# Kernel tuning notes

Hardware: AMD Instinct MI355X
Metric: run time of the kernel (lower is better)

Reference implementation:

```python
import jax, jax.numpy as jnp
import numpy as np

B, L, D = 8, 2048, 1024

def setup_inputs() -> dict:
    key = jax.random.key(0)
    ks = jax.random.split(key, 12)
    s = 1.0 / np.sqrt(D)
    return {
        "q": jax.random.normal(ks[0], (B, L, D), jnp.float32),
        "k": jax.random.normal(ks[1], (B, L, D), jnp.float32),
        "v": jax.random.normal(ks[2], (B, L, D), jnp.float32),
        "mask": jnp.ones((B, L), jnp.float32),
        # Linear params stored as [in, out] so y = x @ W + b
        "Wq": jax.random.normal(ks[3], (D, D), jnp.float32) * s,
        "bq": jnp.zeros((D,), jnp.float32),
        "Wk": jax.random.normal(ks[4], (D, D), jnp.float32) * s,
        "bk": jnp.zeros((D,), jnp.float32),
        "Wv": jax.random.normal(ks[5], (D, D), jnp.float32) * s,
        "bv": jnp.zeros((D,), jnp.float32),
        "Wg": jax.random.normal(ks[6], (2 * D, D), jnp.float32) * (1.0 / np.sqrt(2 * D)),
        "bg": jnp.zeros((D,), jnp.float32),
    }

def reference(q, k, v, mask, Wq, bq, Wk, bk, Wv, bv, Wg, bg):
    q0 = q
    qp = q @ Wq + bq          # [B, Lq, D]
    kp = k @ Wk + bk          # [B, Lk, D]
    vp = v @ Wv + bv          # [B, Lk, D]
    scale = 1.0 / jnp.sqrt(jnp.asarray(qp.shape[-1], qp.dtype))
    w = jnp.einsum('bqd,bkd->bqk', qp, kp) * scale
    w = jax.nn.softmax(w, axis=-1)          # dim=2 == last axis for 3-D
    x = jnp.einsum('bqk,bkd->bqd', w, vp)
    gate = jnp.concatenate((qp, x), axis=-1) @ Wg + bg
    x = x * mask[..., None]
    x = x * jax.nn.sigmoid(gate)
    return x + q0  # add=True
```

## Files before the change

kernel.cpp:

```cpp
#include <hip/hip_runtime.h>

typedef unsigned int u32;
typedef unsigned short u16;
using v4f    = __attribute__((ext_vector_type(4))) float;
using short8 = __attribute__((ext_vector_type(8))) short;

#define GAS __attribute__((address_space(1)))
#define LAS __attribute__((address_space(3)))

__device__ __forceinline__ u16 f2bf(float f){
  u32 u = __builtin_bit_cast(u32, f);
  u32 r = (u + 0x7fffu + ((u >> 16) & 1u)) >> 16;
  return (u16)r;
}
__device__ __forceinline__ float bf2f(u16 h){
  u32 u = ((u32)h) << 16;
  return __builtin_bit_cast(float, u);
}

__device__ __forceinline__ void gld_lds16(const void* g, void* l){
  __builtin_amdgcn_global_load_lds((const GAS u32*)g, (LAS u32*)l, 16, 0, 0);
}

__global__ __launch_bounds__(256) void transpose_w_bf16(
    const float* __restrict__ in, u16* __restrict__ out, int K, int N)
{
  __shared__ float t[64][65];
  const int k0 = blockIdx.x * 64, n0 = blockIdx.y * 64;
  const int tx = threadIdx.x & 63, ty = threadIdx.x >> 6;
  #pragma unroll
  for (int i = 0; i < 16; i++){
    int r = ty + i * 4;
    t[r][tx] = in[(size_t)(k0 + r) * N + (n0 + tx)];
  }
  __syncthreads();
  #pragma unroll
  for (int i = 0; i < 16; i++){
    int r = ty + i * 4;
    out[(size_t)(n0 + r) * K + (k0 + tx)] = f2bf(t[tx][r]);
  }
}

__global__ __launch_bounds__(256) void softmax_rows(u16* __restrict__ S){
  const int lane = threadIdx.x & 63, wid = threadIdx.x >> 6;
  u16* p = S + ((size_t)blockIdx.x * 4 + wid) * 2048;
  uint4 u[4];
  #pragma unroll
  for (int j = 0; j < 4; j++) u[j] = ((const uint4*)p)[lane + j * 64];
  float f[32];
  #pragma unroll
  for (int j = 0; j < 4; j++){
    u32 w4[4] = {u[j].x, u[j].y, u[j].z, u[j].w};
    #pragma unroll
    for (int i = 0; i < 4; i++){
      f[j * 8 + 2*i]     = bf2f((u16)(w4[i] & 0xffffu));
      f[j * 8 + 2*i + 1] = bf2f((u16)(w4[i] >> 16));
    }
  }
  float m = f[0];
  #pragma unroll
  for (int i = 1; i < 32; i++) m = fmaxf(m, f[i]);
  #pragma unroll
  for (int o = 32; o >= 1; o >>= 1) m = fmaxf(m, __shfl_xor(m, o));
  float s = 0.f;
  #pragma unroll
  for (int i = 0; i < 32; i++){ f[i] = __expf(f[i] - m); s += f[i]; }
  #pragma unroll
  for (int o = 32; o >= 1; o >>= 1) s += __shfl_xor(s, o);
  const float inv = 1.f / s;
  #pragma unroll
  for (int j = 0; j < 4; j++){
    u32 w4[4];
    #pragma unroll
    for (int i = 0; i < 4; i++)
      w4[i] = (u32)f2bf(f[j * 8 + 2*i] * inv) |
              ((u32)f2bf(f[j * 8 + 2*i + 1] * inv) << 16);
    ((uint4*)p)[lane + j * 64] = make_uint4(w4[0], w4[1], w4[2], w4[3]);
  }
}

#define BAR() do{ asm volatile("" ::: "memory");                            \
                  __builtin_amdgcn_s_barrier();                             \
                  asm volatile("" ::: "memory"); }while(0)

#define MFMA8(B0, B1, N0, N1)                                               \
    __builtin_amdgcn_s_setprio(1);                                          \
    _Pragma("unroll")                                                       \
    for (int mi = 0; mi < 8; mi++){                                         \
      acc[mi][N0] = __builtin_amdgcn_mfma_f32_16x16x32_bf16(                \
                      a[mi], (B0), acc[mi][N0], 0, 0, 0);                   \
      acc[mi][N1] = __builtin_amdgcn_mfma_f32_16x16x32_bf16(                \
                      a[mi], (B1), acc[mi][N1], 0, 0, 0);                   \
    }                                                                       \
    __builtin_amdgcn_s_setprio(0);

template<int AMODE, int EPI>
__global__ __launch_bounds__(512) void gemm256(
    const float* __restrict__ Af,
    const u16* __restrict__ Ab,
    const u16* __restrict__ A2b,
    const u16* __restrict__ BT,
    int lda, int ldb, int K,
    void* __restrict__ Cout, int ldc,
    const float* __restrict__ bias, float scale,
    size_t aBatch, size_t bBatch, size_t cBatch,
    const u16* __restrict__ xg,
    const float* __restrict__ maskp,
    const float* __restrict__ q0p)
{
  constexpr int BK = 64;
  __shared__ __align__(16) u16 As[2][2][128 * 64];
  __shared__ __align__(16) u16 Bs[2][2][128 * 64];

  const int z   = blockIdx.z;
  const int gx   = (int)gridDim.x;
  const int lin  = (int)blockIdx.y * gx + (int)blockIdx.x;
  const int l2gx = 31 - __clz(gx);
  const int g    = lin >> (3 + l2gx);
  const int rem  = lin & ((gx << 3) - 1);
  const int m0   = ((g << 3) + (rem & 7)) * 256;
  const int n0   = (rem >> 3) * 256;

  const int tid  = (int)threadIdx.x;
  const int lane = tid & 63, wid = tid >> 6;
  const int wm   = (wid >> 2) * 128;
  const int wn   = (wid & 3) * 64;
  const int wnh  = wn >> 7;
  const int wnl  = wn & 127;

  const u16* Az = Ab + (size_t)z * aBatch;
  const u16* Bz = BT + (size_t)z * bBatch;

  u32 offA[2][2], offB[2][2], ldsOff[2];
  #pragma unroll
  for (int i = 0; i < 2; i++){
    int idx = tid + i * 512;
    int r = idx >> 3, c8 = idx & 7;
    int c8s = c8 ^ (r & 7);
    #pragma unroll
    for (int h = 0; h < 2; h++){
      offA[h][i] = (u32)(((m0 + h * 128 + r) * lda + c8s * 8) * 2);
      offB[h][i] = (u32)(((n0 + h * 128 + r) * ldb + c8s * 8) * 2);
    }
    ldsOff[i] = (u32)(idx * 16);
  }

  auto stageQ = [&](int kt, int dbuf, int q){
    const int h = q >> 1, i = q & 1;
    const u32 kb = (u32)(kt * BK * 2);
    if (AMODE != 0){
      const u16* Asrc; u32 ka;
      if (AMODE == 2){
        Asrc = (kt * BK < 1024) ? Az : A2b;
        ka = (u32)(((kt * BK) & 1023) * 2);
      } else {
        Asrc = Az;
        ka = (u32)(kt * BK * 2);
      }
      gld_lds16((const char*)Asrc + offA[h][i] + ka,
                (char*)&As[dbuf][h][0] + ldsOff[i]);
    }
    gld_lds16((const char*)Bz + offB[h][i] + kb,
              (char*)&Bs[dbuf][h][0] + ldsOff[i]);
  };

  v4f afr[2][2][2];
  auto loadA = [&](int kt){
    if (AMODE != 0) return;
    #pragma unroll
    for (int h = 0; h < 2; h++)
      #pragma unroll
      for (int i = 0; i < 2; i++){
        int idx = tid + i * 512;
        int r = idx >> 3, c8s = (idx & 7) ^ (r & 7);
        const float* src = Af + (size_t)(m0 + h * 128 + r) * lda + kt * BK + c8s * 8;
        afr[h][i][0] = ((const v4f*)src)[0];
        afr[h][i][1] = ((const v4f*)src)[1];
      }
  };
  auto writeA = [&](int dbuf){
    if (AMODE != 0) return;
    #pragma unroll
    for (int h = 0; h < 2; h++)
      #pragma unroll
      for (int i = 0; i < 2; i++){
        int idx = tid + i * 512;
        u32 q0 = (u32)f2bf(afr[h][i][0].x) | ((u32)f2bf(afr[h][i][0].y) << 16);
        u32 q1 = (u32)f2bf(afr[h][i][0].z) | ((u32)f2bf(afr[h][i][0].w) << 16);
        u32 q2 = (u32)f2bf(afr[h][i][1].x) | ((u32)f2bf(afr[h][i][1].y) << 16);
        u32 q3 = (u32)f2bf(afr[h][i][1].z) | ((u32)f2bf(afr[h][i][1].w) << 16);
        *(uint4*)((char*)&As[dbuf][h][0] + idx * 16) = make_uint4(q0, q1, q2, q3);
      }
  };

  v4f acc[8][4];
  #pragma unroll
  for (int mi = 0; mi < 8; mi++)
    #pragma unroll
    for (int ni = 0; ni < 4; ni++)
      acc[mi][ni] = (v4f){0.f, 0.f, 0.f, 0.f};

  const int ll  = lane & 15, lq = lane >> 4;
  const int ch0 = ((0 + lq) ^ (ll & 7)) << 3;
  const int ch4 = ((4 + lq) ^ (ll & 7)) << 3;

  if (AMODE == 0){
    loadA(0);
    #pragma unroll
    for (int q = 0; q < 4; q++) stageQ(0, 0, q);
    writeA(0);
  } else {
    #pragma unroll
    for (int q = 0; q < 4; q++) stageQ(0, 0, q);
  }

  const int nt = K / BK;
  for (int kt = 0; kt < nt; kt++){
    const int buf = kt & 1;
    const bool pf = (kt + 1 < nt);

    asm volatile("s_waitcnt vmcnt(0)" ::: "memory");
    if (AMODE == 0) asm volatile("s_waitcnt lgkmcnt(0)" ::: "memory");
    BAR();

    if (pf) loadA(kt + 1);

    const u16* aB = &As[buf][wid >> 2][0] + ll * 64;
    const u16* bB = &Bs[buf][wnh][0] + (wnl + ll) * 64;

    short8 a[8], b[2];
    b[0] = *(const short8*)(bB + ch0);
    b[1] = *(const short8*)(bB + ch0 + 1024);
    #pragma unroll
    for (int mi = 0; mi < 8; mi++) a[mi] = *(const short8*)(aB + ch0 + mi * 1024);
    if (pf) stageQ(kt + 1, buf ^ 1, 0);
    BAR();
    MFMA8(b[0], b[1], 0, 1)
    BAR();
    b[0] = *(const short8*)(bB + ch0 + 2048);
    b[1] = *(const short8*)(bB + ch0 + 3072);
    if (pf) stageQ(kt + 1, buf ^ 1, 1);
    BAR();
    MFMA8(b[0], b[1], 2, 3)
    BAR();
    b[0] = *(const short8*)(bB + ch4);
    b[1] = *(const short8*)(bB + ch4 + 1024);
    #pragma unroll
    for (int mi = 0; mi < 8; mi++) a[mi] = *(const short8*)(aB + ch4 + mi * 1024);
    if (pf) stageQ(kt + 1, buf ^ 1, 2);
    BAR();
    MFMA8(b[0], b[1], 0, 1)
    BAR();
    b[0] = *(const short8*)(bB + ch4 + 2048);
    b[1] = *(const short8*)(bB + ch4 + 3072);
    if (pf) stageQ(kt + 1, buf ^ 1, 3);
    BAR();
    MFMA8(b[0], b[1], 2, 3)
    BAR();

    if (pf) writeA(buf ^ 1);
  }

  const int lr = lq * 4, lc = ll;
  if (EPI == 0 || EPI == 1){
    u16* C = (u16*)Cout + (size_t)z * cBatch;
    #pragma unroll
    for (int mi = 0; mi < 8; mi++){
      #pragma unroll
      for (int ni = 0; ni < 4; ni++){
        int col = n0 + wn + ni * 16 + lc;
        float bv = (EPI == 0) ? bias[col] : 0.f;
        #pragma unroll
        for (int r = 0; r < 4; r++){
          int row = m0 + wm + mi * 16 + lr + r;
          C[(size_t)row * ldc + col] = f2bf(acc[mi][ni][r] * scale + bv);
        }
      }
    }
  } else if (EPI == 3){
    u16* C = (u16*)Cout;
    #pragma unroll
    for (int mi = 0; mi < 8; mi++){
      int rowb = m0 + wm + mi * 16 + lr;
      int bb   = rowb >> 11;
      int rloc = rowb & 2047;
      #pragma unroll
      for (int ni = 0; ni < 4; ni++){
        int col = n0 + wn + ni * 16 + lc;
        float bv = bias[col];
        u32 pk0 = (u32)f2bf(acc[mi][ni][0] + bv) | ((u32)f2bf(acc[mi][ni][1] + bv) << 16);
        u32 pk1 = (u32)f2bf(acc[mi][ni][2] + bv) | ((u32)f2bf(acc[mi][ni][3] + bv) << 16);
        *(uint2*)&C[(size_t)bb * (1024ull * 2048) + (size_t)col * 2048 + rloc] =
            make_uint2(pk0, pk1);
      }
    }
  } else {
    float* C = (float*)Cout;
    #pragma unroll
    for (int mi = 0; mi < 8; mi++){
      #pragma unroll
      for (int ni = 0; ni < 4; ni++){
        int col = n0 + wn + ni * 16 + lc;
        float bv = bias[col];
        #pragma unroll
        for (int r = 0; r < 4; r++){
          int row = m0 + wm + mi * 16 + lr + r;
          float gg = acc[mi][ni][r] + bv;
          float sg = 1.f / (1.f + __expf(-gg));
          float xv = bf2f(xg[(size_t)row * 1024 + col]);
          C[(size_t)row * ldc + col] =
              xv * maskp[row] * sg + q0p[(size_t)row * 1024 + col];
        }
      }
    }
  }
}
#undef MFMA8
#undef BAR

template<int AMODE, int EPI>
__global__ __launch_bounds__(256) void gemm128(
    const float* __restrict__ Af,
    const u16* __restrict__ Ab,
    const u16* __restrict__ A2b,
    const u16* __restrict__ BT,
    int lda, int ldb, int K,
    void* __restrict__ Cout, int ldc,
    const float* __restrict__ bias, float scale,
    size_t aBatch, size_t bBatch, size_t cBatch,
    const u16* __restrict__ xg,
    const float* __restrict__ maskp,
    const float* __restrict__ q0p)
{
  constexpr int BM = 128, BN = 128, BK = 64;
  __shared__ __align__(16) u16 As[BM * BK];
  __shared__ __align__(16) u16 Bs[BN * BK];
  const int z   = blockIdx.z;
  const int lin  = blockIdx.y * gridDim.x + blockIdx.x;
  const int l2gx = 31 - __clz((int)gridDim.x);
  const int g    = lin >> (3 + l2gx);
  const int rem  = lin & (((int)gridDim.x << 3) - 1);
  const int m0   = ((g << 3) + (rem & 7)) * BM;
  const int n0   = (rem >> 3) * BN;
  const int tid = threadIdx.x;
  const int lane = tid & 63, wid = tid >> 6;
  const int wm = (wid >> 1) * 64, wn = (wid & 1) * 64;
  const u16* Abz = Ab + (size_t)z * aBatch;
  const u16* BTz = BT + (size_t)z * bBatch;

  v4f acc[4][4];
  #pragma unroll
  for (int mi = 0; mi < 4; mi++)
    #pragma unroll
    for (int ni = 0; ni < 4; ni++)
      acc[mi][ni] = (v4f){0.f, 0.f, 0.f, 0.f};

  for (int k0 = 0; k0 < K; k0 += BK){
    if (AMODE == 0){
      #pragma unroll
      for (int i = 0; i < 4; i++){
        int idx = tid + i * 256;
        int r = idx >> 3, s = idx & 7;
        const float* src = Af + (size_t)(m0 + r) * lda + (k0 + s * 8);
        v4f lo = ((const v4f*)src)[0];
        v4f hi = ((const v4f*)src)[1];
        u32 p0 = (u32)f2bf(lo.x) | ((u32)f2bf(lo.y) << 16);
        u32 p1 = (u32)f2bf(lo.z) | ((u32)f2bf(lo.w) << 16);
        u32 p2 = (u32)f2bf(hi.x) | ((u32)f2bf(hi.y) << 16);
        u32 p3 = (u32)f2bf(hi.z) | ((u32)f2bf(hi.w) << 16);
        *(uint4*)&As[(size_t)idx * 8] = make_uint4(p0, p1, p2, p3);
      }
    } else {
      #pragma unroll
      for (int i = 0; i < 4; i++){
        int idx = tid + i * 256;
        int r = idx >> 3, s = idx & 7;
        int kk = k0 + s * 8;
        const u16* src;
        if (AMODE == 2){
          src = (kk < 1024) ? (Abz + (size_t)(m0 + r) * 1024 + kk)
                            : (A2b + (size_t)(m0 + r) * 1024 + (kk - 1024));
        } else {
          src = Abz + (size_t)(m0 + r) * lda + kk;
        }
        gld_lds16(src, &As[(size_t)idx * 8]);
      }
    }
    #pragma unroll
    for (int i = 0; i < 4; i++){
      int idx = tid + i * 256;
      int r = idx >> 3, s = idx & 7;
      gld_lds16(BTz + (size_t)(n0 + r) * ldb + (k0 + s * 8), &Bs[(size_t)idx * 8]);
    }
    __syncthreads();
    #pragma unroll
    for (int ks = 0; ks < BK; ks += 32){
      short8 a[4], b[4];
      #pragma unroll
      for (int mi = 0; mi < 4; mi++)
        a[mi] = *(const short8*)&As[(wm + mi * 16 + (lane & 15)) * BK + ks + (lane >> 4) * 8];
      #pragma unroll
      for (int ni = 0; ni < 4; ni++)
        b[ni] = *(const short8*)&Bs[(wn + ni * 16 + (lane & 15)) * BK + ks + (lane >> 4) * 8];
      #pragma unroll
      for (int mi = 0; mi < 4; mi++)
        #pragma unroll
        for (int ni = 0; ni < 4; ni++)
          acc[mi][ni] = __builtin_amdgcn_mfma_f32_16x16x32_bf16(a[mi], b[ni], acc[mi][ni], 0, 0, 0);
    }
    __syncthreads();
  }

  const int lr = (lane >> 4) * 4, lc = lane & 15;
  if (EPI == 0 || EPI == 1){
    u16* C = (u16*)Cout + (size_t)z * cBatch;
    #pragma unroll
    for (int mi = 0; mi < 4; mi++){
      #pragma unroll
      for (int ni = 0; ni < 4; ni++){
        int col = n0 + wn + ni * 16 + lc;
        float bv = (EPI == 0) ? bias[col] : 0.f;
        #pragma unroll
        for (int r = 0; r < 4; r++){
          int row = m0 + wm + mi * 16 + lr + r;
          C[(size_t)row * ldc + col] = f2bf(acc[mi][ni][r] * scale + bv);
        }
      }
    }
  } else if (EPI == 3){
    u16* C = (u16*)Cout;
    #pragma unroll
    for (int mi = 0; mi < 4; mi++){
      int rowb = m0 + wm + mi * 16 + lr;
      int b    = rowb >> 11;
      int rloc = rowb & 2047;
      #pragma unroll
      for (int ni = 0; ni < 4; ni++){
        int col = n0 + wn + ni * 16 + lc;
        float bv = bias[col];
        u32 pk[2];
        pk[0] = (u32)f2bf(acc[mi][ni][0] + bv) | ((u32)f2bf(acc[mi][ni][1] + bv) << 16);
        pk[1] = (u32)f2bf(acc[mi][ni][2] + bv) | ((u32)f2bf(acc[mi][ni][3] + bv) << 16);
        *(uint2*)&C[(size_t)b * (1024ull * 2048) + (size_t)col * 2048 + rloc] =
            make_uint2(pk[0], pk[1]);
      }
    }
  } else {
    float* C = (float*)Cout;
    #pragma unroll
    for (int mi = 0; mi < 4; mi++){
      #pragma unroll
      for (int ni = 0; ni < 4; ni++){
        int col = n0 + wn + ni * 16 + lc;
        float bv = bias[col];
        #pragma unroll
        for (int r = 0; r < 4; r++){
          int row = m0 + wm + mi * 16 + lr + r;
          float g  = acc[mi][ni][r] + bv;
          float sg = 1.f / (1.f + __expf(-g));
          float xv = bf2f(xg[(size_t)row * 1024 + col]);
          C[(size_t)row * ldc + col] =
              xv * maskp[row] * sg + q0p[(size_t)row * 1024 + col];
        }
      }
    }
  }
}

extern "C" void kernel_launch(void* const* d_in, const int* in_sizes, int n_in,
                              void* d_out, int out_size, void* d_ws, size_t ws_size,
                              hipStream_t stream)
{
  const float* q    = (const float*)d_in[0];
  const float* k    = (const float*)d_in[1];
  const float* v    = (const float*)d_in[2];
  const float* mask = (const float*)d_in[3];
  const float* Wq   = (const float*)d_in[4];
  const float* bq   = (const float*)d_in[5];
  const float* Wk   = (const float*)d_in[6];
  const float* bk   = (const float*)d_in[7];
  const float* Wv   = (const float*)d_in[8];
  const float* bv   = (const float*)d_in[9];
  const float* Wg   = (const float*)d_in[10];
  const float* bg   = (const float*)d_in[11];
  float* out = (float*)d_out;

  char* ws = (char*)d_ws;
  const size_t MB = 1024ull * 1024ull;
  u16* WqT = (u16*)(ws + 0 * MB);
  u16* WkT = (u16*)(ws + 2 * MB);
  u16* WvT = (u16*)(ws + 4 * MB);
  u16* WgT = (u16*)(ws + 6 * MB);
  u16* qp  = (u16*)(ws + 10 * MB);
  u16* kp  = (u16*)(ws + 42 * MB);
  u16* vpT = (u16*)(ws + 74 * MB);
  u16* S   = (u16*)(ws + 106 * MB);
  u16* x   = kp;

  const bool bigws = ws_size >= 138 * MB;
  int nb = 8;
  while (nb > 1 && 106 * MB + (size_t)nb * 8 * MB > ws_size) nb >>= 1;
  const int nchunks = 8 / nb;

  dim3 B(256);
  dim3 T5(512);

  transpose_w_bf16<<<dim3(16, 16, 1), B, 0, stream>>>(Wq, WqT, 1024, 1024);
  transpose_w_bf16<<<dim3(16, 16, 1), B, 0, stream>>>(Wk, WkT, 1024, 1024);
  transpose_w_bf16<<<dim3(16, 16, 1), B, 0, stream>>>(Wv, WvT, 1024, 1024);
  transpose_w_bf16<<<dim3(32, 16, 1), B, 0, stream>>>(Wg, WgT, 2048, 1024);

  if (bigws){
    gemm256<0, 0><<<dim3(4, 64, 1), T5, 0, stream>>>(q, nullptr, nullptr, WqT,
        1024, 1024, 1024, qp, 1024, bq, 1.f, 0, 0, 0, nullptr, nullptr, nullptr);
    gemm256<0, 0><<<dim3(4, 64, 1), T5, 0, stream>>>(k, nullptr, nullptr, WkT,
        1024, 1024, 1024, kp, 1024, bk, 1.f, 0, 0, 0, nullptr, nullptr, nullptr);
    gemm256<0, 3><<<dim3(4, 64, 1), T5, 0, stream>>>(v, nullptr, nullptr, WvT,
        1024, 1024, 1024, vpT, 0, bv, 1.f, 0, 0, 0, nullptr, nullptr, nullptr);

    for (int c = 0; c < nchunks; c++){
      const size_t boff = (size_t)c * nb;
      gemm256<1, 1><<<dim3(8, 8, nb), T5, 0, stream>>>(nullptr,
          qp + boff * 2048 * 1024, nullptr, kp + boff * 2048 * 1024,
          1024, 1024, 1024, S, 2048, nullptr, 0.03125f,
          2048ull * 1024, 2048ull * 1024, 2048ull * 2048, nullptr, nullptr, nullptr);
      softmax_rows<<<dim3(nb * 512, 1, 1), B, 0, stream>>>(S);
      gemm256<1, 1><<<dim3(4, 8, nb), T5, 0, stream>>>(nullptr,
          S, nullptr, vpT + boff * 1024 * 2048,
          2048, 2048, 2048, x + boff * 2048 * 1024, 1024, nullptr, 1.f,
          2048ull * 2048, 1024ull * 2048, 2048ull * 1024, nullptr, nullptr, nullptr);
    }

    gemm256<2, 2><<<dim3(4, 64, 1), T5, 0, stream>>>(nullptr, qp, x, WgT,
        1024, 2048, 2048, out, 1024, bg, 1.f, 0, 0, 0, x, mask, q);
  } else {
    gemm128<0, 0><<<dim3(8, 128, 1), B, 0, stream>>>(q, nullptr, nullptr, WqT,
        1024, 1024, 1024, qp, 1024, bq, 1.f, 0, 0, 0, nullptr, nullptr, nullptr);
    gemm128<0, 0><<<dim3(8, 128, 1), B, 0, stream>>>(k, nullptr, nullptr, WkT,
        1024, 1024, 1024, kp, 1024, bk, 1.f, 0, 0, 0, nullptr, nullptr, nullptr);
    gemm128<0, 3><<<dim3(8, 128, 1), B, 0, stream>>>(v, nullptr, nullptr, WvT,
        1024, 1024, 1024, vpT, 0, bv, 1.f, 0, 0, 0, nullptr, nullptr, nullptr);

    for (int c = 0; c < nchunks; c++){
      const size_t boff = (size_t)c * nb;
      gemm128<1, 1><<<dim3(16, 16, nb), B, 0, stream>>>(nullptr,
          qp + boff * 2048 * 1024, nullptr, kp + boff * 2048 * 1024,
          1024, 1024, 1024, S, 2048, nullptr, 0.03125f,
          2048ull * 1024, 2048ull * 1024, 2048ull * 2048, nullptr, nullptr, nullptr);
      softmax_rows<<<dim3(nb * 512, 1, 1), B, 0, stream>>>(S);
      gemm128<1, 1><<<dim3(8, 16, nb), B, 0, stream>>>(nullptr,
          S, nullptr, vpT + boff * 1024 * 2048,
          2048, 2048, 2048, x + boff * 2048 * 1024, 1024, nullptr, 1.f,
          2048ull * 2048, 1024ull * 2048, 2048ull * 1024, nullptr, nullptr, nullptr);
    }

    gemm128<2, 2><<<dim3(8, 128, 1), B, 0, stream>>>(nullptr, qp, x, WgT,
        1024, 2048, 2048, out, 1024, bg, 1.f, 0, 0, 0, x, mask, q);
  }
}
```

Baseline: 662.4 us.

## Drop intra-iteration barriers in gemm256 and issue prefetch once per k-step

Replaces the eight block-wide barriers per k-iteration in the 256-tile GEMM with a single barrier at the top of the loop. All global-to-LDS prefetches for the next tile are now issued immediately after that barrier instead of in four staggered quarters. The fragment loads from shared memory are reordered so B fragments for the next MFMA group are read while the current group computes, with a sched_barrier to fix that ordering. This cuts synchronisation stalls and gives the compiler more room to overlap LDS reads with MFMAs. The cost is more registers for the extra fragment buffers and losing the barrier-enforced interleaving between waves.

```diff
diff --git a/kernel.cpp b/kernel.cpp
--- a/kernel.cpp
+++ b/kernel.cpp
@@ -78,10 +78,6 @@
     ((uint4*)p)[lane + j * 64] = make_uint4(w4[0], w4[1], w4[2], w4[3]);
   }
 }
-
-#define BAR() do{ asm volatile("" ::: "memory");                            \
-                  __builtin_amdgcn_s_barrier();                             \
-                  asm volatile("" ::: "memory"); }while(0)
 
 #define MFMA8(B0, B1, N0, N1)                                               \
     __builtin_amdgcn_s_setprio(1);                                          \
@@ -145,8 +141,7 @@
     ldsOff[i] = (u32)(idx * 16);
   }
 
-  auto stageQ = [&](int kt, int dbuf, int q){
-    const int h = q >> 1, i = q & 1;
+  auto stage = [&](int kt, int dbuf){
     const u32 kb = (u32)(kt * BK * 2);
     if (AMODE != 0){
       const u16* Asrc; u32 ka;
@@ -157,11 +152,19 @@
         Asrc = Az;
         ka = (u32)(kt * BK * 2);
       }
-      gld_lds16((const char*)Asrc + offA[h][i] + ka,
-                (char*)&As[dbuf][h][0] + ldsOff[i]);
-    }
-    gld_lds16((const char*)Bz + offB[h][i] + kb,
-              (char*)&Bs[dbuf][h][0] + ldsOff[i]);
+      #pragma unroll
+      for (int h = 0; h < 2; h++)
+        #pragma unroll
+        for (int i = 0; i < 2; i++)
+          gld_lds16((const char*)Asrc + offA[h][i] + ka,
+                    (char*)&As[dbuf][h][0] + ldsOff[i]);
+    }
+    #pragma unroll
+    for (int h = 0; h < 2; h++)
+      #pragma unroll
+      for (int i = 0; i < 2; i++)
+        gld_lds16((const char*)Bz + offB[h][i] + kb,
+                  (char*)&Bs[dbuf][h][0] + ldsOff[i]);
   };
 
   v4f afr[2][2][2];
@@ -206,12 +209,10 @@
 
   if (AMODE == 0){
     loadA(0);
-    #pragma unroll
-    for (int q = 0; q < 4; q++) stageQ(0, 0, q);
+    stage(0, 0);
     writeA(0);
   } else {
-    #pragma unroll
-    for (int q = 0; q < 4; q++) stageQ(0, 0, q);
+    stage(0, 0);
   }
 
   const int nt = K / BK;
@@ -219,44 +220,37 @@
     const int buf = kt & 1;
     const bool pf = (kt + 1 < nt);
 
+    asm volatile("s_waitcnt lgkmcnt(0)" ::: "memory");
     asm volatile("s_waitcnt vmcnt(0)" ::: "memory");
-    if (AMODE == 0) asm volatile("s_waitcnt lgkmcnt(0)" ::: "memory");
-    BAR();
-
-    if (pf) loadA(kt + 1);
+    __builtin_amdgcn_s_barrier();
+    asm volatile("" ::: "memory");
+
+    if (pf){
+      if (AMODE == 0) loadA(kt + 1);
+      stage(kt + 1, buf ^ 1);
+    }
 
     const u16* aB = &As[buf][wid >> 2][0] + ll * 64;
     const u16* bB = &Bs[buf][wnh][0] + (wnl + ll) * 64;
 
-    short8 a[8], b[2];
-    b[0] = *(const short8*)(bB + ch0);
-    b[1] = *(const short8*)(bB + ch0 + 1024);
+    short8 a[8], b0[2], b1[2], p0[2], p1[2];
+    b0[0] = *(const short8*)(bB + ch0);
+    b0[1] = *(const short8*)(bB + ch0 + 1024);
     #pragma unroll
     for (int mi = 0; mi < 8; mi++) a[mi] = *(const short8*)(aB + ch0 + mi * 1024);
-    if (pf) stageQ(kt + 1, buf ^ 1, 0);
-    BAR();
-    MFMA8(b[0], b[1], 0, 1)
-    BAR();
-    b[0] = *(const short8*)(bB + ch0 + 2048);
-    b[1] = *(const short8*)(bB + ch0 + 3072);
-    if (pf) stageQ(kt + 1, buf ^ 1, 1);
-    BAR();
-    MFMA8(b[0], b[1], 2, 3)
-    BAR();
-    b[0] = *(const short8*)(bB + ch4);
-    b[1] = *(const short8*)(bB + ch4 + 1024);
+    b1[0] = *(const short8*)(bB + ch0 + 2048);
+    b1[1] = *(const short8*)(bB + ch0 + 3072);
+    MFMA8(b0[0], b0[1], 0, 1)
+    p0[0] = *(const short8*)(bB + ch4);
+    p0[1] = *(const short8*)(bB + ch4 + 1024);
+    MFMA8(b1[0], b1[1], 2, 3)
+    p1[0] = *(const short8*)(bB + ch4 + 2048);
+    p1[1] = *(const short8*)(bB + ch4 + 3072);
+    __builtin_amdgcn_sched_barrier(0);
     #pragma unroll
     for (int mi = 0; mi < 8; mi++) a[mi] = *(const short8*)(aB + ch4 + mi * 1024);
-    if (pf) stageQ(kt + 1, buf ^ 1, 2);
-    BAR();
-    MFMA8(b[0], b[1], 0, 1)
-    BAR();
-    b[0] = *(const short8*)(bB + ch4 + 2048);
-    b[1] = *(const short8*)(bB + ch4 + 3072);
-    if (pf) stageQ(kt + 1, buf ^ 1, 3);
-    BAR();
-    MFMA8(b[0], b[1], 2, 3)
-    BAR();
+    MFMA8(p0[0], p0[1], 0, 1)
+    MFMA8(p1[0], p1[1], 2, 3)
 
     if (pf) writeA(buf ^ 1);
   }
@@ -316,7 +310,6 @@
   }
 }
 #undef MFMA8
-#undef BAR
 
 template<int AMODE, int EPI>
 __global__ __launch_bounds__(256) void gemm128(
```

Measured after the change: 625.7 us. 5.5% less time.
